# Kernel tuning notes

Hardware: AMD Instinct MI355X
Metric: run time of the kernel (lower is better)

Reference implementation:

```python
import jax, jax.numpy as jnp
import numpy as np
from jax import lax

IN_CH, FEAT, EMB, P = 384, 256, 32, 64
OUT_CH = (256, 512, 1024, 1024)
EPS_BN = 1e-5


def _conv(x, w, b, stride=1, pad=1, groups=1):
    # x: (B,C,H,W), w: (O, C//groups, kh, kw) torch OIHW layout
    y = lax.conv_general_dilated(x, w, (stride, stride), ((pad, pad), (pad, pad)),
                                 dimension_numbers=('NCHW', 'OIHW', 'NCHW'),
                                 feature_group_count=groups)
    return y + b[None, :, None, None]


def _bn(x, g, b, m, v):
    scale = (g / jnp.sqrt(v + EPS_BN))[None, :, None, None]
    return (x - m[None, :, None, None]) * scale + b[None, :, None, None]


def _convT_block(x, w, b, k):
    # ConvTranspose2d with kernel_size == stride == k, padding 0 (non-overlapping)
    # w: (C_in, C_out, k, k) torch layout
    B, C, H, W = x.shape
    O = w.shape[1]
    y = jnp.einsum('bchw,coij->bohiwj', x, w).reshape(B, O, H * k, W * k)
    return y + b[None, :, None, None]


def _resize_ac(x, oh, ow):
    # bilinear interpolation, align_corners=True; x: (B,C,H,W)
    H, W = x.shape[-2], x.shape[-1]
    def idx(n_in, n_out):
        c = jnp.arange(n_out, dtype=x.dtype) * ((n_in - 1) / max(n_out - 1, 1))
        i0 = jnp.clip(jnp.floor(c).astype(jnp.int32), 0, max(n_in - 2, 0))
        return i0, c - i0.astype(x.dtype)
    if oh != H:
        i0, t = idx(H, oh)
        x = x[:, :, i0, :] * (1.0 - t)[:, None] + x[:, :, jnp.minimum(i0 + 1, H - 1), :] * t[:, None]
    if ow != W:
        j0, t = idx(W, ow)
        x = x[:, :, :, j0] * (1.0 - t) + x[:, :, :, jnp.minimum(j0 + 1, W - 1)] * t
    return x


def _avg3(x):
    # F.avg_pool2d(k=3, s=1, p=1) with count_include_pad=True -> always /9
    s = lax.reduce_window(x, jnp.float32(0.0), lax.add, (1, 1, 3, 3), (1, 1, 1, 1),
                          ((0, 0), (0, 0), (1, 1), (1, 1)))
    return s / 9.0


def _forward(tokens0, tokens1, tokens2, tokens3,
             proj_w0, proj_b0, proj_w1, proj_b1, proj_w2, proj_b2, proj_w3, proj_b3,
             up_w0, up_b0, up_w1, up_b1, down_w3, down_b3,
             fuse_w, fuse_b,
             pe_w1, pe_b1, pe_bn_g, pe_bn_b, pe_bn_m, pe_bn_v, pe_w2, pe_b2,
             prototypes, prototype_biases, bias_scale,
             smooth_w, smooth_b,
             head_w1, head_b1, hbn1_g, hbn1_b, hbn1_m, hbn1_v,
             head_w2, head_b2, hbn2_g, hbn2_b, hbn2_m, hbn2_v,
             head_w3, head_b3, residual_scale,
             patch_h, patch_w):
    B = tokens0.shape[0]
    toks = (tokens0, tokens1, tokens2, tokens3)
    proj = ((proj_w0, proj_b0), (proj_w1, proj_b1), (proj_w2, proj_b2), (proj_w3, proj_b3))
    feats = []
    for t, (w, b) in zip(toks, proj):
        x = t.transpose(0, 2, 1).reshape(B, t.shape[-1], patch_h, patch_w)
        x = jnp.einsum('bchw,oc->bohw', x, w[:, :, 0, 0]) + b[None, :, None, None]  # 1x1 proj
        feats.append(x)
    f0 = _convT_block(feats[0], up_w0, up_b0, 4)
    f1 = _convT_block(feats[1], up_w1, up_b1, 2)
    f2 = feats[2]                                         # identity
    f3 = _conv(feats[3], down_w3, down_b3, stride=2)
    th, tw = f0.shape[-2], f0.shape[-1]
    fused = jnp.concatenate([f0, _resize_ac(f1, th, tw), _resize_ac(f2, th, tw), _resize_ac(f3, th, tw)], axis=1)
    path1 = jax.nn.relu(jnp.einsum('bchw,oc->bohw', fused, fuse_w[:, :, 0, 0]) + fuse_b[None, :, None, None])
    H, W = patch_h * 14, patch_w * 14
    path1 = _resize_ac(path1, H, W)
    pe = _conv(path1, pe_w1, pe_b1)
    pe = jax.nn.relu(_bn(pe, pe_bn_g, pe_bn_b, pe_bn_m, pe_bn_v))
    pe = _conv(pe, pe_w2, pe_b2)                          # (B, EMB, H, W)
    sim = jnp.einsum('behw,pe->bphw', pe, prototypes) / jnp.sqrt(jnp.float32(pe.shape[1]))
    # edge map from embedding gradients, replicate-padded
    gx = jnp.abs(pe[:, :, :, :-1] - pe[:, :, :, 1:])
    gy = jnp.abs(pe[:, :, :-1, :] - pe[:, :, 1:, :])
    gx = jnp.concatenate([gx, gx[:, :, :, -1:]], axis=3)
    gy = jnp.concatenate([gy, gy[:, :, -1:, :]], axis=2)
    edge = (gx.mean(axis=1, keepdims=True) + gy.mean(axis=1, keepdims=True)) * 0.5
    mask = (edge > edge.mean()).astype(pe.dtype)
    for _ in range(2):  # fixed 2-step edge-aware smoothing
        sim = mask * sim + (1.0 - mask) * _avg3(sim)
    # first softmax over prototypes -> entropy regularizer
    act1 = jax.nn.softmax(sim, axis=1)
    activation_entropy = -(act1 * jnp.log(act1 + 1e-8)).sum(axis=1).mean()
    # spatial smoothing conv then second softmax over prototypes
    sim = _conv(sim, smooth_w, smooth_b)
    act = jax.nn.softmax(sim, axis=1)                     # (B, P, H, W)
    bb = 1.0 + jnp.tanh(prototype_biases) * bias_scale    # (P,)
    base_biases = jnp.broadcast_to(bb[None, :], (B, bb.shape[0]))
    base_gain = jnp.einsum('bphw,p->bhw', act, bb)[:, None]  # (B,1,H,W)
    # 64 per-prototype residual heads == grouped convs with groups=P
    n_proto = act.shape[1]
    h = jax.nn.relu(_bn(_conv(act, head_w1, head_b1, groups=n_proto), hbn1_g, hbn1_b, hbn1_m, hbn1_v))
    h = jax.nn.relu(_bn(_conv(h, head_w2, head_b2, groups=n_proto), hbn2_g, hbn2_b, hbn2_m, hbn2_v))
    res = _conv(h, head_w3, head_b3, groups=n_proto)      # (B, P, H, W)
    weighted = (act * res).sum(axis=1, keepdims=True)
    gain = base_gain * (1.0 + jnp.tanh(weighted) * residual_scale)
    instance_bias_map = jnp.clip(gain, 0.5, 2.0)
    return instance_bias_map, act, base_biases, weighted, pe, activation_entropy


def setup_inputs() -> dict:
    key = jax.random.key(0)
    B, N, PH, PW = 2, 256, 16, 16
    ks = iter(jax.random.split(key, 48))
    def rnd(shape, s=1.0):
        return jax.random.normal(next(ks), shape, dtype=jnp.float32) * s
    inp = {}
    for i in range(4):
        inp['tokens%d' % i] = rnd((B, N, IN_CH))
    for i, oc in enumerate(OUT_CH):
        inp['proj_w%d' % i] = rnd((oc, IN_CH, 1, 1), 0.02)
        inp['proj_b%d' % i] = rnd((oc,), 0.01)
    inp['up_w0'] = rnd((OUT_CH[0], OUT_CH[0], 4, 4), 0.02)
    inp['up_b0'] = rnd((OUT_CH[0],), 0.01)
    inp['up_w1'] = rnd((OUT_CH[1], OUT_CH[1], 2, 2), 0.02)
    inp['up_b1'] = rnd((OUT_CH[1],), 0.01)
    inp['down_w3'] = rnd((OUT_CH[3], OUT_CH[3], 3, 3), 0.01)
    inp['down_b3'] = rnd((OUT_CH[3],), 0.01)
    inp['fuse_w'] = rnd((FEAT, sum(OUT_CH), 1, 1), 0.01)
    inp['fuse_b'] = rnd((FEAT,), 0.01)
    inp['pe_w1'] = rnd((FEAT // 2, FEAT, 3, 3), 0.02)
    inp['pe_b1'] = rnd((FEAT // 2,), 0.01)
    inp['pe_bn_g'] = 1.0 + rnd((FEAT // 2,), 0.1)
    inp['pe_bn_b'] = rnd((FEAT // 2,), 0.01)
    inp['pe_bn_m'] = rnd((FEAT // 2,), 0.01)
    inp['pe_bn_v'] = jnp.ones((FEAT // 2,), jnp.float32)
    inp['pe_w2'] = rnd((EMB, FEAT // 2, 3, 3), 0.02)
    inp['pe_b2'] = rnd((EMB,), 0.01)
    inp['prototypes'] = rnd((P, EMB), 0.01)
    inp['prototype_biases'] = rnd((P,), 0.1)
    inp['bias_scale'] = jnp.asarray(0.2, jnp.float32)
    inp['smooth_w'] = rnd((P, P, 3, 3), 0.02)
    inp['smooth_b'] = rnd((P,), 0.01)
    inp['head_w1'] = rnd((P * 8, 1, 3, 3), 0.1)
    inp['head_b1'] = rnd((P * 8,), 0.01)
    inp['hbn1_g'] = 1.0 + rnd((P * 8,), 0.1)
    inp['hbn1_b'] = rnd((P * 8,), 0.01)
    inp['hbn1_m'] = rnd((P * 8,), 0.01)
    inp['hbn1_v'] = jnp.ones((P * 8,), jnp.float32)
    inp['head_w2'] = rnd((P * 8, 8, 3, 3), 0.1)
    inp['head_b2'] = rnd((P * 8,), 0.01)
    inp['hbn2_g'] = 1.0 + rnd((P * 8,), 0.1)
    inp['hbn2_b'] = rnd((P * 8,), 0.01)
    inp['hbn2_m'] = rnd((P * 8,), 0.01)
    inp['hbn2_v'] = jnp.ones((P * 8,), jnp.float32)
    inp['head_w3'] = rnd((P, 8, 3, 3), 0.1)
    inp['head_b3'] = rnd((P,), 0.01)
    inp['residual_scale'] = jnp.asarray(0.1, jnp.float32)
    inp['patch_h'] = PH
    inp['patch_w'] = PW
    return inp


def reference(tokens0, tokens1, tokens2, tokens3,
              proj_w0, proj_b0, proj_w1, proj_b1, proj_w2, proj_b2, proj_w3, proj_b3,
              up_w0, up_b0, up_w1, up_b1, down_w3, down_b3,
              fuse_w, fuse_b,
              pe_w1, pe_b1, pe_bn_g, pe_bn_b, pe_bn_m, pe_bn_v, pe_w2, pe_b2,
              prototypes, prototype_biases, bias_scale,
              smooth_w, smooth_b,
              head_w1, head_b1, hbn1_g, hbn1_b, hbn1_m, hbn1_v,
              head_w2, head_b2, hbn2_g, hbn2_b, hbn2_m, hbn2_v,
              head_w3, head_b3, residual_scale,
              patch_h, patch_w):
    return _forward(tokens0, tokens1, tokens2, tokens3,
                    proj_w0, proj_b0, proj_w1, proj_b1, proj_w2, proj_b2, proj_w3, proj_b3,
                    up_w0, up_b0, up_w1, up_b1, down_w3, down_b3,
                    fuse_w, fuse_b,
                    pe_w1, pe_b1, pe_bn_g, pe_bn_b, pe_bn_m, pe_bn_v, pe_w2, pe_b2,
                    prototypes, prototype_biases, bias_scale,
                    smooth_w, smooth_b,
                    head_w1, head_b1, hbn1_g, hbn1_b, hbn1_m, hbn1_v,
                    head_w2, head_b2, hbn2_g, hbn2_b, hbn2_m, hbn2_v,
                    head_w3, head_b3, residual_scale,
                    patch_h, patch_w)
```

## Files before the change

kernel.cpp:

```cpp
#include <hip/hip_runtime.h>
#include <math.h>

#define BATCH 2
#define NTOK 256
#define INCH 384
#define NP 50176
#define HW 224
#define NPROTO 64
#define EMBD 32

#define OFF_FEATS0   0u
#define OFF_FEATS1   131072u
#define OFF_FEATS2   393216u
#define OFF_FEATS3   917504u
#define OFF_TOKT     1441792u
#define OFF_F0       2228224u
#define OFF_F1       4325376u
#define OFF_F3       5373952u
#define OFF_FUSEDBF  5505024u
#define OFF_WD       5505024u
#define OFF_PART     14942208u
#define OFF_P64C     28573696u
#define OFF_P224C    0u
#define OFF_T1       25690112u
#define OFF_PC2      0u
#define OFF_SIMRAW   25690112u
#define OFF_PSM      25690112u
#define OFF_SIMA     0u
#define OFF_EDGE     12845056u
#define OFF_RES      13000000u
#define OFF_WB       13000000u
#define OFF_SHIFT    13200000u
#define OFF_BGAIN    19422528u
#define OFF_BB       19522880u
#define OFF_ACC      19523008u
#define OFF_WF       19523072u
#define OFF_WFUSE    20000000u
#define OFF_WCV0     20500000u
#define OFF_WCV1     21600000u
#define OFF_WC2      22700000u
#define OFF_WSM      22750000u

#define O_IBM 0u
#define O_ACT 100352u
#define O_BB  6522880u
#define O_WT  6523008u
#define O_PE  6623360u
#define O_ENT 9834624u

typedef __attribute__((ext_vector_type(8))) short bf16x8;
typedef __attribute__((ext_vector_type(4))) float f32x4;
typedef __attribute__((ext_vector_type(2))) float f32x2;

__device__ __forceinline__ short f2bf(float f) {
    unsigned u = __float_as_uint(f);
    unsigned r = (u + 0x7fffu + ((u >> 16) & 1u)) >> 16;
    return (short)r;
}
__device__ __forceinline__ float bf2f(short s) {
    return __uint_as_float(((unsigned)(unsigned short)s) << 16);
}

__global__ void k_transpose(const float* __restrict__ in, float* __restrict__ out) {
    int idx = blockIdx.x * 256 + threadIdx.x;
    int n = idx & 255;
    int c = (idx >> 8) % INCH;
    int b = idx / (INCH * NTOK);
    out[idx] = in[(size_t)b * INCH * NTOK + (size_t)n * INCH + c];
}

__global__ __launch_bounds__(256) void k_proj(const float* __restrict__ A,
                                              const float* __restrict__ W,
                                              const float* __restrict__ bias,
                                              float* __restrict__ out, int O) {
    int p = threadIdx.x;
    int o = blockIdx.x, b = blockIdx.y;
    const float* a = A + (size_t)b * INCH * NTOK + p;
    const float* w = W + (size_t)o * INCH;
    float acc = bias[o];
    for (int c = 0; c < INCH; ++c) acc = fmaf(a[(size_t)c * NTOK], w[c], acc);
    out[((size_t)b * O + o) * NTOK + p] = acc;
}

template <int NT>
__global__ __launch_bounds__(256) void k_wcvprep(const float* __restrict__ W,
                                                 float* __restrict__ WP, int C, int M) {
    __shared__ float t[32][33];
    int c0 = blockIdx.x * 32, m0 = blockIdx.y * 32;
    int tx = threadIdx.x & 31, ty = threadIdx.x >> 5;
#pragma unroll
    for (int r = 0; r < 4; ++r) {
        int cl = ty + r * 8;
        t[cl][tx] = W[(size_t)(c0 + cl) * M + m0 + tx];
    }
    __syncthreads();
    for (int i = threadIdx.x; i < 1024; i += 256) {
        int ml = i % NT;
        int tmp = i / NT;
        int cl = tmp & 31;
        int mh = tmp >> 5;
        WP[(size_t)(m0 / NT + mh) * C * NT + (size_t)(c0 + cl) * NT + ml] = t[cl][mh * NT + ml];
    }
}

template <int NT, int CCH, int K>
__global__ __launch_bounds__(256) void k_convt2(const float* __restrict__ X,
                                                const float* __restrict__ WP,
                                                const float* __restrict__ bias,
                                                float* __restrict__ out,
                                                int C, int O) {
    __shared__ float sX[CCH * 256];
    int tid = threadIdx.x;
    int nt = blockIdx.x, b = blockIdx.y;
    float acc[NT];
#pragma unroll
    for (int j = 0; j < NT; ++j) acc[j] = 0.f;
    const float* Xb = X + (size_t)b * C * 256;
    for (int cc = 0; cc < C; cc += CCH) {
        __syncthreads();
        const f32x4* Xg4 = (const f32x4*)(Xb + (size_t)cc * 256);
        f32x4* s4 = (f32x4*)sX;
        for (int i = tid; i < CCH * 64; i += 256) s4[i] = Xg4[i];
        __syncthreads();
        const float* wr = WP + ((size_t)nt * C + cc) * NT;
        for (int c = 0; c < CCH; ++c) {
            float xv = sX[c * 256 + tid];
            const float* w = wr + c * NT;
#pragma unroll
            for (int j = 0; j < NT; ++j) acc[j] = fmaf(xv, w[j], acc[j]);
        }
    }
    int h = tid >> 4, w = tid & 15;
    int S = 16 * K;
#pragma unroll
    for (int j = 0; j < NT; ++j) {
        int m = nt * NT + j;
        int o = m / (K * K);
        int ij = m - o * (K * K);
        int ii = ij / K, jj = ij - ii * K;
        out[((size_t)b * O + o) * (size_t)(S * S) + (h * K + ii) * S + (w * K + jj)] =
            acc[j] + bias[o];
    }
}

__global__ __launch_bounds__(256) void k_wdprep(const float* __restrict__ W,
                                                float* __restrict__ WP) {
    __shared__ float t[32][33];
    int k0 = blockIdx.x * 32, o0 = blockIdx.y * 32;
    int tx = threadIdx.x & 31, ty = threadIdx.x >> 5;
#pragma unroll
    for (int r = 0; r < 4; ++r) {
        int orow = ty + r * 8;
        t[orow][tx] = W[(size_t)(o0 + orow) * 9216 + k0 + tx];
    }
    __syncthreads();
#pragma unroll
    for (int r = 0; r < 4; ++r) {
        int krow = ty + r * 8;
        int o = o0 + tx;
        WP[(size_t)(o >> 6) * 589824 + (size_t)(k0 + krow) * 64 + (o & 63)] = t[tx][krow];
    }
}

__global__ __launch_bounds__(256) void k_down2(const float* __restrict__ X,
                                               const float* __restrict__ WP,
                                               float* __restrict__ part) {
    __shared__ float sX[64 * 256];
    int tid = threadIdx.x;
    int ot = blockIdx.x, kc = blockIdx.y, b = blockIdx.z;
    int c0 = kc * 64;
    const float* Xg = X + ((size_t)b * 1024 + c0) * 256;
    for (int i = tid; i < 16384; i += 256) {
        int c = i >> 8, px = i & 255;
        int sy = px >> 4, sx = px & 15;
        int par = (sy & 1) * 2 + (sx & 1);
        sX[(c * 4 + par) * 64 + (sy >> 1) * 8 + (sx >> 1)] = Xg[i];
    }
    __syncthreads();
    int lane = tid & 63;
    int w = __builtin_amdgcn_readfirstlane(tid >> 6);
    int oh = lane >> 3, ow = lane & 7;
    int loff[9]; float lmsk[9];
#pragma unroll
    for (int kh = 0; kh < 3; ++kh)
#pragma unroll
        for (int kw = 0; kw < 3; ++kw) {
            int py = (kh == 1) ? 0 : 1;
            int pxp = (kw == 1) ? 0 : 1;
            int u = oh - ((kh == 0) ? 1 : 0);
            int v = ow - ((kw == 0) ? 1 : 0);
            float m = (u >= 0 && v >= 0) ? 1.f : 0.f;
            if (u < 0) u = 0;
            if (v < 0) v = 0;
            loff[kh * 3 + kw] = (py * 2 + pxp) * 64 + u * 8 + v;
            lmsk[kh * 3 + kw] = m;
        }
    float acc[16];
#pragma unroll
    for (int j = 0; j < 16; ++j) acc[j] = 0.f;
    const float* wb = WP + (size_t)ot * 589824 + (size_t)c0 * 576 + w * 16;
    for (int c = 0; c < 64; ++c) {
        const float* xb = sX + c * 256;
        const float* wc = wb + (size_t)c * 576;
#pragma unroll
        for (int tap = 0; tap < 9; ++tap) {
            float xv = xb[loff[tap]] * lmsk[tap];
            const float* wr = wc + tap * 64;
#pragma unroll
            for (int j = 0; j < 16; ++j) acc[j] = fmaf(xv, wr[j], acc[j]);
        }
    }
    float* pp = part + ((size_t)((kc * 2 + b) * 1024 + ot * 64 + w * 16)) * 64 + lane;
#pragma unroll
    for (int j = 0; j < 16; ++j) pp[(size_t)j * 64] = acc[j];
}

__global__ __launch_bounds__(256) void k_downred(const float* __restrict__ part,
                                                 const float* __restrict__ bias,
                                                 float* __restrict__ out) {
    int idx = blockIdx.x * 256 + threadIdx.x;
    int o = (idx >> 6) & 1023;
    int b = idx >> 16;
    int px = idx & 63;
    float s = bias[o];
#pragma unroll
    for (int kcs = 0; kcs < 16; ++kcs)
        s += part[((size_t)(kcs * 2 + b) * 1024 + o) * 64 + px];
    out[idx] = s;
}

__global__ void k_fusedcat_bf(const float* __restrict__ f0, const float* __restrict__ f1,
                              const float* __restrict__ f2, const float* __restrict__ f3,
                              short* __restrict__ out) {
    int idx = blockIdx.x * 256 + threadIdx.x;
    int ch = idx % 2816;
    int t = idx / 2816;
    int pos = t & 4095;
    int b = t >> 12;
    float v;
    if (ch < 256) {
        v = f0[((size_t)(b * 256 + ch)) * 4096 + pos];
    } else {
        const float* src; int sh;
        if (ch < 768)       { src = f1 + ((size_t)(b * 512 + (ch - 256))) * 1024; sh = 32; }
        else if (ch < 1792) { src = f2 + ((size_t)(b * 1024 + (ch - 768))) * 256; sh = 16; }
        else                { src = f3 + ((size_t)(b * 1024 + (ch - 1792))) * 64; sh = 8;  }
        int y = pos >> 6, x = pos & 63;
        float r = (float)(sh - 1) / 63.0f;
        float cy = y * r, cx = x * r;
        int i0 = (int)cy; if (i0 > sh - 2) i0 = sh - 2;
        int j0 = (int)cx; if (j0 > sh - 2) j0 = sh - 2;
        float ty = cy - (float)i0, tx = cx - (float)j0;
        const float* s0 = src + i0 * sh + j0;
        float v00 = s0[0], v01 = s0[1], v10 = s0[sh], v11 = s0[sh + 1];
        float c0 = v00 + ty * (v10 - v00);
        float c1 = v01 + ty * (v11 - v01);
        v = c0 + tx * (c1 - c0);
    }
    out[idx] = f2bf(v);
}

__global__ void k_wfuseprep(const float* __restrict__ w, short* __restrict__ wb) {
    int idx = blockIdx.x * 256 + threadIdx.x;
    int j = idx & 7;
    int lane = (idx >> 3) & 63;
    int ntile = (idx >> 9) & 15;
    int chunk = idx >> 13;
    int oc = ntile * 16 + (lane & 15);
    int c = chunk * 32 + (lane >> 4) * 8 + j;
    wb[idx] = f2bf(w[(size_t)oc * 2816 + c]);
}

__global__ __launch_bounds__(256) void k_fuse_mfma(const short* __restrict__ A,
                                                   const bf16x8* __restrict__ WB,
                                                   const float* __restrict__ bias,
                                                   short* __restrict__ out) {
    int tid = threadIdx.x;
    int lane = tid & 63, w = tid >> 6;
    int row0 = blockIdx.x * 16;
    int l15 = lane & 15, q = lane >> 4;
    int arow = row0 + l15;
    f32x4 acc[4];
#pragma unroll
    for (int nn = 0; nn < 4; ++nn) acc[nn] = (f32x4){0.f, 0.f, 0.f, 0.f};
    const short* arp = A + (size_t)arow * 2816 + q * 8;
    for (int chunk = 0; chunk < 88; ++chunk) {
        bf16x8 a = *(const bf16x8*)(arp + chunk * 32);
        const bf16x8* wbp = WB + ((size_t)(chunk * 16 + w * 4) * 64) + lane;
#pragma unroll
        for (int nn = 0; nn < 4; ++nn) {
            bf16x8 bf = wbp[nn * 64];
            acc[nn] = __builtin_amdgcn_mfma_f32_16x16x32_bf16(a, bf, acc[nn], 0, 0, 0);
        }
    }
#pragma unroll
    for (int nn = 0; nn < 4; ++nn) {
        int oc = (w * 4 + nn) * 16 + l15;
        float bs = bias[oc];
#pragma unroll
        for (int r = 0; r < 4; ++r) {
            int m = q * 4 + r;
            out[(size_t)(row0 + m) * 256 + oc] = f2bf(fmaxf(acc[nn][r] + bs, 0.f));
        }
    }
}

__global__ void k_resize224bf2(const short* __restrict__ in, short* __restrict__ out) {
    int idx = blockIdx.x * 256 + threadIdx.x;
    int c8 = (idx & 31) * 8;
    int p = idx >> 5;
    int b = p / NP;
    int pos = p - b * NP;
    int y = pos / HW, x = pos - y * HW;
    const float r = (float)(63.0 / 223.0);
    float cy = y * r, cx = x * r;
    int i0 = (int)cy; if (i0 > 62) i0 = 62;
    int j0 = (int)cx; if (j0 > 62) j0 = 62;
    float ty = cy - (float)i0, tx = cx - (float)j0;
    const short* base = in + ((size_t)b * 4096) * 256 + c8;
    const bf16x8 v00 = *(const bf16x8*)(base + (size_t)(i0 * 64 + j0) * 256);
    const bf16x8 v01 = *(const bf16x8*)(base + (size_t)(i0 * 64 + j0 + 1) * 256);
    const bf16x8 v10 = *(const bf16x8*)(base + (size_t)((i0 + 1) * 64 + j0) * 256);
    const bf16x8 v11 = *(const bf16x8*)(base + (size_t)((i0 + 1) * 64 + j0 + 1) * 256);
    bf16x8 o;
#pragma unroll
    for (int k = 0; k < 8; ++k) {
        float a00 = bf2f(v00[k]), a01 = bf2f(v01[k]);
        float a10 = bf2f(v10[k]), a11 = bf2f(v11[k]);
        float c0 = a00 + ty * (a10 - a00);
        float c1 = a01 + ty * (a11 - a01);
        o[k] = f2bf(c0 + tx * (c1 - c0));
    }
    *(bf16x8*)(out + ((size_t)b * NP + pos) * 256 + c8) = o;
}

__global__ void k_w1prep(const float* __restrict__ w, const float* __restrict__ bias,
                         const float* __restrict__ g, const float* __restrict__ bb,
                         const float* __restrict__ m, const float* __restrict__ v,
                         short* __restrict__ wb, float* __restrict__ shift) {
    int idx = blockIdx.x * 256 + threadIdx.x;
    int j = idx & 7;
    int lane = (idx >> 3) & 63;
    int nt = (idx >> 9) & 7;
    int tc = idx >> 12;
    int tap = tc % 9, chunk = tc / 9;
    int oc = nt * 16 + (lane & 15);
    int c = chunk * 32 + (lane >> 4) * 8 + j;
    float s = g[oc] * rsqrtf(v[oc] + 1e-5f);
    wb[idx] = f2bf(w[((size_t)oc * 256 + c) * 9 + tap] * s);
    if (idx < 128) {
        float si = g[idx] * rsqrtf(v[idx] + 1e-5f);
        shift[idx] = (bias[idx] - m[idx]) * si + bb[idx];
    }
}

__global__ __launch_bounds__(256) void k_conv1mfma(const short* __restrict__ X,
                                                   const bf16x8* __restrict__ WB,
                                                   const float* __restrict__ shift,
                                                   float* __restrict__ out) {
    int tid = threadIdx.x;
    int lane = tid & 63, w = tid >> 6;
    int t = blockIdx.x;
    int b = blockIdx.y;
    int ty0 = (t / 28) * 8, tx0 = (t % 28) * 8;
    int l15 = lane & 15, q = lane >> 4;
    int loc = w * 16 + l15;
    int py0 = ty0 + (loc >> 3), px0 = tx0 + (loc & 7);
    int csub = q * 8;
    f32x4 acc0[8];
#pragma unroll
    for (int nt = 0; nt < 8; ++nt) acc0[nt] = (f32x4){0.f, 0.f, 0.f, 0.f};
    const short* Xb = X + (size_t)b * NP * 256;
    const bf16x8 zv = {0, 0, 0, 0, 0, 0, 0, 0};
    for (int chunk = 0; chunk < 8; ++chunk) {
        int c0 = chunk * 32 + csub;
#pragma unroll
        for (int tap = 0; tap < 9; ++tap) {
            int dy = tap / 3 - 1, dx = tap % 3 - 1;
            int sy0 = py0 + dy, sx0 = px0 + dx;
            bf16x8 a0 = zv;
            if ((unsigned)sy0 < HW && (unsigned)sx0 < HW)
                a0 = *(const bf16x8*)(Xb + ((size_t)sy0 * HW + sx0) * 256 + c0);
            const bf16x8* wbp = WB + (size_t)((chunk * 9 + tap) * 8) * 64 + lane;
#pragma unroll
            for (int nt = 0; nt < 8; ++nt) {
                bf16x8 bf = wbp[nt * 64];
                acc0[nt] = __builtin_amdgcn_mfma_f32_16x16x32_bf16(a0, bf, acc0[nt], 0, 0, 0);
            }
        }
    }
#pragma unroll
    for (int nt = 0; nt < 8; ++nt) {
        int oc = nt * 16 + l15;
        float sh = shift[oc];
        float* ob = out + ((size_t)(b * 128 + oc)) * NP;
#pragma unroll
        for (int r = 0; r < 4; ++r) {
            int lm = w * 16 + q * 4 + r;
            int py = ty0 + (lm >> 3), px = tx0 + (lm & 7);
            ob[py * HW + px] = fmaxf(acc0[nt][r] + sh, 0.f);
        }
    }
}

__global__ void k_wc3prep(const float* __restrict__ W, float* __restrict__ WP,
                          int C, int O) {
    int idx = blockIdx.x * 256 + threadIdx.x;
    if (idx >= C * 9 * O) return;
    int o = idx % O;
    int t = idx / O;
    int tap = t % 9, c = t / 9;
    WP[idx] = W[((size_t)o * C + c) * 9 + tap];
}

template <int O, int CB>
__global__ __launch_bounds__(256) void k_conv3v3(const float* __restrict__ in,
                                                 const float* __restrict__ WP,
                                                 float* __restrict__ part, int C) {
    __shared__ float sX[8 * 360];
    int tid = threadIdx.x;
    int tb = blockIdx.x, s = blockIdx.y, b = blockIdx.z;
    int ty0 = (tb / 7) * 8, tx0 = (tb % 7) * 32;
    int px = tid & 31, py = tid >> 5;
    float acc[O];
#pragma unroll
    for (int o = 0; o < O; ++o) acc[o] = 0.f;
    int c0 = s * CB;
    const float* ic = in + ((size_t)b * C + c0) * NP;
    const float* wbase = WP + (size_t)c0 * 9 * O;
    for (int cc = 0; cc < CB; cc += 8) {
        __syncthreads();
        for (int i = tid; i < 8 * 340; i += 256) {
            int c = i / 340;
            int r = i - c * 340;
            int y = r / 34, x = r - y * 34;
            int sy = ty0 + y - 1, sx = tx0 + x - 1;
            float v = 0.f;
            if ((unsigned)sy < HW && (unsigned)sx < HW)
                v = ic[(size_t)(cc + c) * NP + sy * HW + sx];
            sX[c * 360 + y * 36 + x] = v;
        }
        __syncthreads();
        const float* xb = sX + py * 36 + px;
#pragma unroll 1
        for (int c = 0; c < 8; ++c) {
            const float* xc = xb + c * 360;
            const float* wc = wbase + (size_t)(cc + c) * 9 * O;
#pragma unroll
            for (int kh = 0; kh < 3; ++kh)
#pragma unroll
                for (int kw = 0; kw < 3; ++kw) {
                    float xv = xc[kh * 36 + kw];
                    const float* wt = wc + (kh * 3 + kw) * O;
#pragma unroll
                    for (int o = 0; o < O; ++o) acc[o] = fmaf(xv, wt[o], acc[o]);
                }
        }
    }
    int gy = ty0 + py, gx = tx0 + px;
    float* ob = part + ((size_t)(s * BATCH + b) * O) * NP + (size_t)gy * HW + gx;
#pragma unroll
    for (int o = 0; o < O; ++o) ob[(size_t)o * NP] = acc[o];
}

__global__ __launch_bounds__(256) void k_red32sim(const float* __restrict__ part,
                                                  const float* __restrict__ bias,
                                                  const float* __restrict__ proto,
                                                  float* __restrict__ o_pe,
                                                  float* __restrict__ simout) {
    int idx = blockIdx.x * 256 + threadIdx.x;
    int b = idx / NP, pos = idx - b * NP;
    float v[32];
#pragma unroll
    for (int o = 0; o < 32; ++o) {
        float s = bias[o];
#pragma unroll
        for (int s2 = 0; s2 < 4; ++s2)
            s += part[((size_t)((s2 * BATCH + b) * 32 + o)) * NP + pos];
        v[o] = s;
        o_pe[((size_t)(b * 32 + o)) * NP + pos] = s;
    }
    const float scale = 1.0f / sqrtf(32.0f);
    float* so = simout + (size_t)b * NPROTO * NP + pos;
    for (int q = 0; q < NPROTO; ++q) {
        float acc = 0.f;
#pragma unroll
        for (int e = 0; e < 32; ++e) acc = fmaf(v[e], proto[q * EMBD + e], acc);
        so[(size_t)q * NP] = acc * scale;
    }
}

__global__ void k_init(float* acc) { if (threadIdx.x < 8) acc[threadIdx.x] = 0.f; }

__device__ __forceinline__ float block_reduce_sum(float v) {
    __shared__ float sh[4];
#pragma unroll
    for (int off = 32; off > 0; off >>= 1) v += __shfl_down(v, off);
    int lane = threadIdx.x & 63, wv = threadIdx.x >> 6;
    if (lane == 0) sh[wv] = v;
    __syncthreads();
    return (threadIdx.x == 0) ? (sh[0] + sh[1] + sh[2] + sh[3]) : 0.f;
}

__global__ __launch_bounds__(256) void k_edge(const float* __restrict__ pe,
                                              float* __restrict__ edge,
                                              float* __restrict__ acc) {
    int idx = blockIdx.x * 256 + threadIdx.x;
    int b = idx / NP, pos = idx - b * NP;
    int h = pos / HW, w = pos - h * HW;
    int wn = (w < HW - 1) ? w : HW - 2;
    int hn = (h < HW - 1) ? h : HW - 2;
    const float* pb = pe + (size_t)b * EMBD * NP;
    float sx = 0.f, sy = 0.f;
#pragma unroll 4
    for (int e = 0; e < EMBD; ++e) {
        const float* p = pb + (size_t)e * NP;
        sx += fabsf(p[h * HW + wn] - p[h * HW + wn + 1]);
        sy += fabsf(p[hn * HW + w] - p[hn * HW + HW + w]);
    }
    float ev = (sx + sy) * (0.5f / 32.0f);
    edge[idx] = ev;
    float tot = block_reduce_sum(ev);
    if (threadIdx.x == 0) atomicAdd(acc, tot);
}

__global__ __launch_bounds__(256) void k_smooth2x(const float* __restrict__ sin_,
                                                  const float* __restrict__ edge,
                                                  const float* __restrict__ acc,
                                                  float* __restrict__ sout) {
    __shared__ float sIn[20 * 20];
    __shared__ float sE[18 * 18];
    __shared__ float s1[18 * 18];
    int tid = threadIdx.x;
    int tile = blockIdx.x, p = blockIdx.y, b = blockIdx.z;
    int oy0 = (tile / 14) * 16, ox0 = (tile % 14) * 16;
    float mean = acc[0] * (1.0f / 100352.0f);
    const float* sc = sin_ + ((size_t)(b * NPROTO + p)) * NP;
    const float* eb = edge + (size_t)b * NP;
    for (int i = tid; i < 400; i += 256) {
        int y = i / 20, x = i - y * 20;
        int gy = oy0 - 2 + y, gx = ox0 - 2 + x;
        float v = 0.f;
        if ((unsigned)gy < HW && (unsigned)gx < HW) v = sc[gy * HW + gx];
        sIn[i] = v;
    }
    for (int i = tid; i < 324; i += 256) {
        int y = i / 18, x = i - y * 18;
        int gy = oy0 - 1 + y, gx = ox0 - 1 + x;
        float e = 0.f;
        if ((unsigned)gy < HW && (unsigned)gx < HW) e = eb[gy * HW + gx];
        sE[i] = e;
    }
    __syncthreads();
    for (int i = tid; i < 324; i += 256) {
        int y = i / 18, x = i - y * 18;
        int gy = oy0 - 1 + y, gx = ox0 - 1 + x;
        float r = 0.f;
        if ((unsigned)gy < HW && (unsigned)gx < HW) {
            const float* c0 = sIn + (y + 1) * 20 + (x + 1);
            float s = c0[-21] + c0[-20] + c0[-19]
                    + c0[-1]  + c0[0]   + c0[1]
                    + c0[19]  + c0[20]  + c0[21];
            float m = (sE[i] > mean) ? 1.f : 0.f;
            r = m * c0[0] + (1.f - m) * (s * (1.0f / 9.0f));
        }
        s1[i] = r;
    }
    __syncthreads();
    {
        int px = tid & 15, py = tid >> 4;
        int gy = oy0 + py, gx = ox0 + px;
        const float* c1 = s1 + (py + 1) * 18 + (px + 1);
        float s = c1[-19] + c1[-18] + c1[-17]
                + c1[-1]  + c1[0]   + c1[1]
                + c1[17]  + c1[18]  + c1[19];
        float m = (sE[(py + 1) * 18 + (px + 1)] > mean) ? 1.f : 0.f;
        sout[((size_t)(b * NPROTO + p)) * NP + (size_t)gy * HW + gx] =
            m * c1[0] + (1.f - m) * (s * (1.0f / 9.0f));
    }
}

__global__ __launch_bounds__(256) void k_entropy(const float* __restrict__ sim,
                                                 float* __restrict__ acc) {
    int idx = blockIdx.x * 256 + threadIdx.x;
    int b = idx / NP, pos = idx - b * NP;
    const float* s = sim + (size_t)b * NPROTO * NP + pos;
    float v[NPROTO];
    float mx = -3.0e38f;
#pragma unroll
    for (int q = 0; q < NPROTO; ++q) { v[q] = s[(size_t)q * NP]; mx = fmaxf(mx, v[q]); }
    float sum = 0.f;
#pragma unroll
    for (int q = 0; q < NPROTO; ++q) { float e = expf(v[q] - mx); v[q] = e; sum += e; }
    float inv = 1.f / sum;
    float ent = 0.f;
#pragma unroll
    for (int q = 0; q < NPROTO; ++q) {
        float a = v[q] * inv;
        ent -= a * logf(a + 1e-8f);
    }
    float tot = block_reduce_sum(ent);
    if (threadIdx.x == 0) atomicAdd(acc + 1, tot);
}

__global__ void k_bb(const float* __restrict__ pb, const float* __restrict__ bs,
                     float* __restrict__ bbuf, float* __restrict__ obb) {
    int t = threadIdx.x;
    if (t < NPROTO) {
        float v = 1.f + tanhf(pb[t]) * bs[0];
        bbuf[t] = v;
        obb[t] = v;
        obb[NPROTO + t] = v;
    }
}

__global__ __launch_bounds__(256) void k_actsm2(const float* __restrict__ part,
                                                const float* __restrict__ bias,
                                                const float* __restrict__ bb,
                                                float* __restrict__ act,
                                                float* __restrict__ bgain) {
    int idx = blockIdx.x * 256 + threadIdx.x;
    int b = idx / NP, pos = idx - b * NP;
    float v[NPROTO];
    float mx = -3.0e38f;
#pragma unroll
    for (int q = 0; q < NPROTO; ++q) {
        float s = bias[q];
        s += part[((size_t)((0 * BATCH + b) * NPROTO + q)) * NP + pos];
        s += part[((size_t)((1 * BATCH + b) * NPROTO + q)) * NP + pos];
        v[q] = s;
        mx = fmaxf(mx, s);
    }
    float sum = 0.f;
#pragma unroll
    for (int q = 0; q < NPROTO; ++q) { float e = expf(v[q] - mx); v[q] = e; sum += e; }
    float inv = 1.f / sum;
    float* a = act + (size_t)b * NPROTO * NP + pos;
    float bg = 0.f;
#pragma unroll
    for (int q = 0; q < NPROTO; ++q) {
        float p = v[q] * inv;
        a[(size_t)q * NP] = p;
        bg = fmaf(p, bb[q], bg);
    }
    bgain[idx] = bg;
}

__global__ void k_headprep(const float* __restrict__ w1, const float* __restrict__ b1,
                           const float* __restrict__ g1, const float* __restrict__ be1,
                           const float* __restrict__ m1, const float* __restrict__ v1,
                           const float* __restrict__ w2, const float* __restrict__ b2,
                           const float* __restrict__ g2, const float* __restrict__ be2,
                           const float* __restrict__ m2, const float* __restrict__ v2,
                           float* __restrict__ wf) {
    int oc = blockIdx.x * 256 + threadIdx.x;
    if (oc >= 512) return;
    float s1 = g1[oc] * rsqrtf(v1[oc] + 1e-5f);
#pragma unroll
    for (int k = 0; k < 9; ++k) wf[oc * 9 + k] = w1[oc * 9 + k] * s1;
    wf[41472 + oc] = (b1[oc] - m1[oc]) * s1 + be1[oc];
    float s2 = g2[oc] * rsqrtf(v2[oc] + 1e-5f);
    int g = oc >> 3, j = oc & 7;
#pragma unroll
    for (int icc = 0; icc < 8; ++icc)
#pragma unroll
        for (int k = 0; k < 9; ++k)
            wf[4608 + (size_t)g * 576 + icc * 72 + j * 9 + k] = w2[((size_t)oc * 8 + icc) * 9 + k] * s2;
    wf[41984 + oc] = (b2[oc] - m2[oc]) * s2 + be2[oc];
}

__global__ __launch_bounds__(256) void k_heads(
    const float* __restrict__ act, const float* __restrict__ wf,
    const float* __restrict__ w3, const float* __restrict__ b3,
    float* __restrict__ res) {
    __shared__ float sA[22 * 24];
    __shared__ float sH1[8][20 * 22];
    __shared__ float sH2[8][18 * 18];
    int tid = threadIdx.x;
    int tile = blockIdx.x, g = blockIdx.y, b = blockIdx.z;
    int oy0 = (tile / 14) * 16, ox0 = (tile % 14) * 16;
    const float* ain = act + (size_t)(b * NPROTO + g) * NP;

    for (int i = tid; i < 484; i += 256) {
        int y = i / 22, x = i - y * 22;
        int gy = oy0 - 3 + y, gx = ox0 - 3 + x;
        float v = 0.f;
        if ((unsigned)gy < HW && (unsigned)gx < HW) v = ain[gy * HW + gx];
        sA[y * 24 + x] = v;
    }
    __syncthreads();

    const float* b1f = wf + 41472 + g * 8;
    for (int i = tid; i < 400; i += 256) {
        int y = i / 20, x = i - y * 20;
        int gy = oy0 - 2 + y, gx = ox0 - 2 + x;
        float keep = ((unsigned)gy < HW && (unsigned)gx < HW) ? 1.f : 0.f;
        const float* s0 = sA + y * 24 + x;
        float r0 = s0[0],  r1 = s0[1],  r2 = s0[2];
        float r3 = s0[24], r4 = s0[25], r5 = s0[26];
        float r6 = s0[48], r7 = s0[49], r8 = s0[50];
#pragma unroll
        for (int j = 0; j < 8; ++j) {
            const float* w = wf + (g * 8 + j) * 9;
            float v = fmaf(r0, w[0], fmaf(r1, w[1], fmaf(r2, w[2],
                      fmaf(r3, w[3], fmaf(r4, w[4], fmaf(r5, w[5],
                      fmaf(r6, w[6], fmaf(r7, w[7], fmaf(r8, w[8], b1f[j])))))))));
            sH1[j][y * 22 + x] = fmaxf(v, 0.f) * keep;
        }
    }
    __syncthreads();

    const float* w2f = wf + 4608 + (size_t)g * 576;
    const float* b2f = wf + 41984 + g * 8;
    if (tid < 162) {
        int y2 = tid / 9, xp = (tid - y2 * 9) * 2;
        f32x2 a2[8];
#pragma unroll
        for (int j = 0; j < 8; ++j) { float bv = b2f[j]; a2[j] = (f32x2){bv, bv}; }
#pragma unroll
        for (int icc = 0; icc < 8; ++icc) {
            const float* s0 = &sH1[icc][y2 * 22 + xp];
            f32x2 t[9];
#pragma unroll
            for (int r = 0; r < 3; ++r) {
                float f0 = s0[r * 22], f1 = s0[r * 22 + 1];
                float f2 = s0[r * 22 + 2], f3 = s0[r * 22 + 3];
                t[r * 3 + 0] = (f32x2){f0, f1};
                t[r * 3 + 1] = (f32x2){f1, f2};
                t[r * 3 + 2] = (f32x2){f2, f3};
            }
            const float* wr = w2f + icc * 72;
#pragma unroll
            for (int j = 0; j < 8; ++j) {
                const float* wj = wr + j * 9;
#pragma unroll
                for (int k = 0; k < 9; ++k) {
                    float wv = wj[k];
                    a2[j] = __builtin_elementwise_fma(t[k], (f32x2){wv, wv}, a2[j]);
                }
            }
        }
        int gy = oy0 - 1 + y2;
        int gx0 = ox0 - 1 + xp;
        float k0 = ((unsigned)gy < HW && (unsigned)gx0 < HW) ? 1.f : 0.f;
        float k1 = ((unsigned)gy < HW && (unsigned)(gx0 + 1) < HW) ? 1.f : 0.f;
        f32x2 kp = (f32x2){k0, k1};
        const f32x2 z2 = (f32x2){0.f, 0.f};
#pragma unroll
        for (int j = 0; j < 8; ++j) {
            f32x2 v = __builtin_elementwise_max(a2[j], z2) * kp;
            sH2[j][y2 * 18 + xp] = v.x;
            sH2[j][y2 * 18 + xp + 1] = v.y;
        }
    }
    __syncthreads();

    if (tid < 128) {
        int y3 = tid >> 3, xp = (tid & 7) * 2;
        float bv = b3[g];
        f32x2 a2 = (f32x2){bv, bv};
#pragma unroll
        for (int icc = 0; icc < 8; ++icc) {
            const float* s0 = &sH2[icc][y3 * 18 + xp];
            const float* w = w3 + (size_t)(g * 8 + icc) * 9;
#pragma unroll
            for (int r = 0; r < 3; ++r) {
                float f0 = s0[r * 18], f1 = s0[r * 18 + 1];
                float f2 = s0[r * 18 + 2], f3 = s0[r * 18 + 3];
                float w0 = w[r * 3], w1 = w[r * 3 + 1], w2v = w[r * 3 + 2];
                a2 = __builtin_elementwise_fma((f32x2){f0, f1}, (f32x2){w0, w0}, a2);
                a2 = __builtin_elementwise_fma((f32x2){f1, f2}, (f32x2){w1, w1}, a2);
                a2 = __builtin_elementwise_fma((f32x2){f2, f3}, (f32x2){w2v, w2v}, a2);
            }
        }
        float* rp = res + (size_t)(b * NPROTO + g) * NP + (size_t)(oy0 + y3) * HW + (ox0 + xp);
        rp[0] = a2.x;
        rp[1] = a2.y;
    }
}

__global__ __launch_bounds__(256) void k_final(const float* __restrict__ act,
                                               const float* __restrict__ res,
                                               const float* __restrict__ bgain,
                                               const float* __restrict__ rscale,
                                               float* __restrict__ owt,
                                               float* __restrict__ oibm) {
    int idx = blockIdx.x * 256 + threadIdx.x;
    int b = idx / NP, pos = idx - b * NP;
    const float* a = act + (size_t)b * NPROTO * NP + pos;
    const float* r = res + (size_t)b * NPROTO * NP + pos;
    float wt = 0.f;
#pragma unroll
    for (int q = 0; q < NPROTO; ++q) wt = fmaf(a[(size_t)q * NP], r[(size_t)q * NP], wt);
    owt[idx] = wt;
    float gn = bgain[idx] * (1.f + tanhf(wt) * rscale[0]);
    gn = fminf(fmaxf(gn, 0.5f), 2.0f);
    oibm[idx] = gn;
}

__global__ void k_entfinal(const float* __restrict__ acc, float* __restrict__ o) {
    if (threadIdx.x == 0) o[0] = acc[1] * (1.0f / 100352.0f);
}

extern "C" void kernel_launch(void* const* d_in, const int* in_sizes, int n_in,
                              void* d_out, int out_size, void* d_ws, size_t ws_size,
                              hipStream_t stream) {
    const float* tokens[4] = {(const float*)d_in[0], (const float*)d_in[1],
                              (const float*)d_in[2], (const float*)d_in[3]};
    const float* proj_w[4] = {(const float*)d_in[4], (const float*)d_in[6],
                              (const float*)d_in[8], (const float*)d_in[10]};
    const float* proj_b[4] = {(const float*)d_in[5], (const float*)d_in[7],
                              (const float*)d_in[9], (const float*)d_in[11]};
    const float* up_w0 = (const float*)d_in[12]; const float* up_b0 = (const float*)d_in[13];
    const float* up_w1 = (const float*)d_in[14]; const float* up_b1 = (const float*)d_in[15];
    const float* down_w3 = (const float*)d_in[16]; const float* down_b3 = (const float*)d_in[17];
    const float* fuse_w = (const float*)d_in[18]; const float* fuse_b = (const float*)d_in[19];
    const float* pe_w1 = (const float*)d_in[20]; const float* pe_b1 = (const float*)d_in[21];
    const float* pe_bn_g = (const float*)d_in[22]; const float* pe_bn_b = (const float*)d_in[23];
    const float* pe_bn_m = (const float*)d_in[24]; const float* pe_bn_v = (const float*)d_in[25];
    const float* pe_w2 = (const float*)d_in[26]; const float* pe_b2 = (const float*)d_in[27];
    const float* prototypes = (const float*)d_in[28];
    const float* proto_biases = (const float*)d_in[29];
    const float* bias_scale = (const float*)d_in[30];
    const float* smooth_w = (const float*)d_in[31]; const float* smooth_b = (const float*)d_in[32];
    const float* hw1 = (const float*)d_in[33]; const float* hb1 = (const float*)d_in[34];
    const float* hg1 = (const float*)d_in[35]; const float* hbe1 = (const float*)d_in[36];
    const float* hm1 = (const float*)d_in[37]; const float* hv1 = (const float*)d_in[38];
    const float* hw2 = (const float*)d_in[39]; const float* hb2 = (const float*)d_in[40];
    const float* hg2 = (const float*)d_in[41]; const float* hbe2 = (const float*)d_in[42];
    const float* hm2 = (const float*)d_in[43]; const float* hv2 = (const float*)d_in[44];
    const float* hw3 = (const float*)d_in[45]; const float* hb3 = (const float*)d_in[46];
    const float* rscale = (const float*)d_in[47];
    (void)in_sizes; (void)n_in; (void)out_size; (void)ws_size;

    float* ws = (float*)d_ws;
    float* FEATS[4] = {ws + OFF_FEATS0, ws + OFF_FEATS1, ws + OFF_FEATS2, ws + OFF_FEATS3};
    float* TOKT = ws + OFF_TOKT;
    float* F0 = ws + OFF_F0; float* F1 = ws + OFF_F1; float* F3 = ws + OFF_F3;
    short* FUSEDBF = (short*)(ws + OFF_FUSEDBF);
    short* P64C = (short*)(ws + OFF_P64C);
    short* P224C = (short*)(ws + OFF_P224C);
    short* WB = (short*)(ws + OFF_WB);
    short* WFUSE = (short*)(ws + OFF_WFUSE);
    float* SHIFT = ws + OFF_SHIFT;
    float* T1 = ws + OFF_T1;
    float* SIMA = ws + OFF_SIMA;
    float* SIMRAW = ws + OFF_SIMRAW;
    float* EDGE = ws + OFF_EDGE; float* RES = ws + OFF_RES;
    float* BGAIN = ws + OFF_BGAIN; float* BBUF = ws + OFF_BB; float* ACC = ws + OFF_ACC;
    float* WF = ws + OFF_WF;
    float* WDP = ws + OFF_WD;
    float* PART = ws + OFF_PART;
    float* WCV0 = ws + OFF_WCV0;
    float* WCV1 = ws + OFF_WCV1;
    float* WC2 = ws + OFF_WC2;
    float* WSM = ws + OFF_WSM;
    float* PC2 = ws + OFF_PC2;
    float* PSM = ws + OFF_PSM;

    float* out = (float*)d_out;
    float* o_ibm = out + O_IBM; float* o_act = out + O_ACT; float* o_bb = out + O_BB;
    float* o_wt = out + O_WT; float* o_pe = out + O_PE; float* o_ent = out + O_ENT;

    const int OCH[4] = {256, 512, 1024, 1024};
    for (int s = 0; s < 4; ++s)
        k_transpose<<<768, 256, 0, stream>>>(tokens[s], TOKT + s * 196608);
    for (int s = 0; s < 4; ++s)
        k_proj<<<dim3(OCH[s], BATCH), 256, 0, stream>>>(TOKT + s * 196608, proj_w[s], proj_b[s],
                                                        FEATS[s], OCH[s]);
    k_wcvprep<16><<<dim3(8, 128), 256, 0, stream>>>(up_w0, WCV0, 256, 4096);
    k_wcvprep<8><<<dim3(16, 64), 256, 0, stream>>>(up_w1, WCV1, 512, 2048);
    k_convt2<16, 64, 4><<<dim3(256, BATCH), 256, 0, stream>>>(FEATS[0], WCV0, up_b0, F0, 256, 256);
    k_convt2<8, 64, 2><<<dim3(256, BATCH), 256, 0, stream>>>(FEATS[1], WCV1, up_b1, F1, 512, 512);
    k_wdprep<<<dim3(288, 32), 256, 0, stream>>>(down_w3, WDP);
    k_down2<<<dim3(16, 16, BATCH), 256, 0, stream>>>(FEATS[3], WDP, PART);
    k_downred<<<512, 256, 0, stream>>>(PART, down_b3, F3);
    k_wc3prep<<<144, 256, 0, stream>>>(pe_w2, WC2, 128, 32);
    k_wc3prep<<<144, 256, 0, stream>>>(smooth_w, WSM, 64, 64);
    k_wfuseprep<<<2816, 256, 0, stream>>>(fuse_w, WFUSE);
    k_fusedcat_bf<<<90112, 256, 0, stream>>>(F0, F1, FEATS[2], F3, FUSEDBF);
    k_fuse_mfma<<<512, 256, 0, stream>>>(FUSEDBF, (const bf16x8*)WFUSE, fuse_b, P64C);
    k_w1prep<<<1152, 256, 0, stream>>>(pe_w1, pe_b1, pe_bn_g, pe_bn_b, pe_bn_m, pe_bn_v,
                                       WB, SHIFT);
    k_resize224bf2<<<12544, 256, 0, stream>>>(P64C, P224C);
    k_conv1mfma<<<dim3(784, BATCH), 256, 0, stream>>>(P224C, (const bf16x8*)WB, SHIFT, T1);
    k_conv3v3<32, 32><<<dim3(196, 4, BATCH), 256, 0, stream>>>(T1, WC2, PC2, 128);
    k_red32sim<<<392, 256, 0, stream>>>(PC2, pe_b2, prototypes, o_pe, SIMRAW);
    k_init<<<1, 64, 0, stream>>>(ACC);
    k_edge<<<392, 256, 0, stream>>>(o_pe, EDGE, ACC);
    k_smooth2x<<<dim3(196, NPROTO, BATCH), 256, 0, stream>>>(SIMRAW, EDGE, ACC, SIMA);
    k_entropy<<<392, 256, 0, stream>>>(SIMA, ACC);
    k_conv3v3<64, 32><<<dim3(196, 2, BATCH), 256, 0, stream>>>(SIMA, WSM, PSM, 64);
    k_bb<<<1, 64, 0, stream>>>(proto_biases, bias_scale, BBUF, o_bb);
    k_actsm2<<<392, 256, 0, stream>>>(PSM, smooth_b, BBUF, o_act, BGAIN);
    k_headprep<<<2, 256, 0, stream>>>(hw1, hb1, hg1, hbe1, hm1, hv1,
                                      hw2, hb2, hg2, hbe2, hm2, hv2, WF);
    k_heads<<<dim3(196, 64, BATCH), 256, 0, stream>>>(o_act, WF, hw3, hb3, RES);
    k_final<<<392, 256, 0, stream>>>(o_act, RES, BGAIN, rscale, o_wt, o_ibm);
    k_entfinal<<<1, 1, 0, stream>>>(ACC, o_ent);
}
```

Measured before the change: 1.526 ms.

## Stage conv1 weights through LDS and prefetch next tap's operands

The 3x3 conv MFMA kernel previously had every wave load its own copy of the 8 weight fragments from global memory for each chunk/tap. Now the block loads each 512-entry weight slice once into shared memory and all four waves read it from there. The next iteration's weights and input vector are prefetched into registers while the current MFMAs run. This cuts redundant global weight traffic and hides load latency, at the cost of two __syncthreads per iteration and a flattened, non-unrolled loop.

```diff
diff --git a/kernel.cpp b/kernel.cpp
--- a/kernel.cpp
+++ b/kernel.cpp
@@ -358,6 +358,7 @@
                                                    const bf16x8* __restrict__ WB,
                                                    const float* __restrict__ shift,
                                                    float* __restrict__ out) {
+    __shared__ bf16x8 wl[512];
     int tid = threadIdx.x;
     int lane = tid & 63, w = tid >> 6;
     int t = blockIdx.x;
@@ -372,22 +373,39 @@
     for (int nt = 0; nt < 8; ++nt) acc0[nt] = (f32x4){0.f, 0.f, 0.f, 0.f};
     const short* Xb = X + (size_t)b * NP * 256;
     const bf16x8 zv = {0, 0, 0, 0, 0, 0, 0, 0};
-    for (int chunk = 0; chunk < 8; ++chunk) {
-        int c0 = chunk * 32 + csub;
-#pragma unroll
-        for (int tap = 0; tap < 9; ++tap) {
-            int dy = tap / 3 - 1, dx = tap % 3 - 1;
-            int sy0 = py0 + dy, sx0 = px0 + dx;
-            bf16x8 a0 = zv;
-            if ((unsigned)sy0 < HW && (unsigned)sx0 < HW)
-                a0 = *(const bf16x8*)(Xb + ((size_t)sy0 * HW + sx0) * 256 + c0);
-            const bf16x8* wbp = WB + (size_t)((chunk * 9 + tap) * 8) * 64 + lane;
-#pragma unroll
-            for (int nt = 0; nt < 8; ++nt) {
-                bf16x8 bf = wbp[nt * 64];
-                acc0[nt] = __builtin_amdgcn_mfma_f32_16x16x32_bf16(a0, bf, acc0[nt], 0, 0, 0);
-            }
-        }
+    bf16x8 na = WB[tid];
+    bf16x8 nb = WB[256 + tid];
+    wl[tid] = na;
+    wl[tid + 256] = nb;
+    bf16x8 a_cur = zv;
+    {
+        int sy = py0 - 1, sx = px0 - 1;
+        if ((unsigned)sy < HW && (unsigned)sx < HW)
+            a_cur = *(const bf16x8*)(Xb + ((size_t)sy * HW + sx) * 256 + csub);
+    }
+    for (int it = 0; it < 72; ++it) {
+        __syncthreads();
+        bf16x8 a_nxt = zv;
+        if (it < 71) {
+            na = WB[(it + 1) * 512 + tid];
+            nb = WB[(it + 1) * 512 + 256 + tid];
+            int itn = it + 1;
+            int cn = itn / 9, tn = itn - cn * 9;
+            int sy = py0 + tn / 3 - 1, sx = px0 + (tn % 3) - 1;
+            if ((unsigned)sy < HW && (unsigned)sx < HW)
+                a_nxt = *(const bf16x8*)(Xb + ((size_t)sy * HW + sx) * 256 + cn * 32 + csub);
+        }
+#pragma unroll
+        for (int nt = 0; nt < 8; ++nt) {
+            bf16x8 bf = wl[nt * 64 + lane];
+            acc0[nt] = __builtin_amdgcn_mfma_f32_16x16x32_bf16(a_cur, bf, acc0[nt], 0, 0, 0);
+        }
+        __syncthreads();
+        if (it < 71) {
+            wl[tid] = na;
+            wl[tid + 256] = nb;
+        }
+        a_cur = a_nxt;
     }
 #pragma unroll
     for (int nt = 0; nt < 8; ++nt) {
```

After: 1.448 ms. 1.05x faster.
